# Kernel optimization log

Measured on AMD Instinct MI355X. Metric: run time of the kernel, lower is better.

## Reference

```python
import jax, jax.numpy as jnp
import numpy as np

GRID_RES_SAMPLE = 0.08  # config.grid_resolution_sample
VOXEL_SIZE = 0.04       # scene voxel size encoded in transforms


def setup_inputs() -> dict:
    key = jax.random.key(0)
    ks = jax.random.split(key, 4)
    B, X = 4, 96
    G = 192            # == ceil(X * GRID_RES_SAMPLE / VOXEL_SIZE), matches dynamic size_voxel_grid
    N = 500_000        # sparse occupied voxels per scene
    NUM_ADD = 5000     # static stand-in for occ_grids.sum()+100 mask augmentations
    # scene voxel-grid transform: scale VOXEL_SIZE, translate -5m (same structure per scene)
    T = np.eye(4, dtype=np.float32)
    T[0, 0] = T[1, 1] = T[2, 2] = VOXEL_SIZE
    T[:3, 3] = -5.0
    transforms = np.tile(T, (B, 1, 1)).astype(np.float32)
    transforms_inv = np.stack([np.linalg.inv(t) for t in transforms]).astype(np.float32)
    # per-batch regular coordinate grids with random world offsets in [0,1)m
    offs = np.asarray(jax.random.uniform(ks[0], (B, 3), dtype=jnp.float32))
    ax = np.arange(X, dtype=np.float32) * GRID_RES_SAMPLE
    gx, gy, gz = np.meshgrid(ax, ax, ax, indexing='ij')
    base = np.stack([gx, gy, gz], axis=0)  # [3,X,X,X]
    coords = (base[None] + offs[:, :, None, None, None]).astype(np.float32)
    sparse = jax.random.randint(ks[1], (B, N, 3), 0, 400, dtype=jnp.int32)
    rand_idx = jax.random.randint(ks[2], (3, NUM_ADD), 0, X, dtype=jnp.int32)
    conv_w = jnp.ones((1, 1, 5, 5, 5), jnp.float32)  # Conv3d(1,1,5) all-ones, no bias
    return {
        'coordinate_grids': jnp.asarray(coords),
        'transforms': jnp.asarray(transforms),
        'transforms_inv': jnp.asarray(transforms_inv),
        'sparse_encoding': sparse,
        'conv_w': conv_w,
        'rand_idx': rand_idx,
        'grid_size': G,
    }


def reference(coordinate_grids, transforms, transforms_inv, sparse_encoding, conv_w, rand_idx, grid_size):
    B, C, X, Y, Z = coordinate_grids.shape
    flat = coordinate_grids.reshape(B, 3, -1)
    min_loc = flat.min(-1)   # [B,3]
    max_loc = flat.max(-1)   # [B,3]
    max_size_grid = (max_loc + GRID_RES_SAMPLE - min_loc).max(0)  # [3]
    min_homo = jnp.concatenate([min_loc, jnp.ones((B, 1), flat.dtype)], axis=1)
    min_voxel_idx = jnp.floor(jnp.einsum('bij,bj->bi', transforms_inv, min_homo)[:, :3])
    min_voxel_idx = jnp.maximum(min_voxel_idx, 0.0)  # [B,3]
    size_vox = jnp.ceil(jnp.einsum('bij,j->bi', transforms_inv[:, :3, :3], max_size_grid).max(0))  # [3], == grid_size
    # shift sparse indices into the local window and filter out-of-range ones
    se = sparse_encoding.astype(jnp.float32) - min_voxel_idx[:, None, :]   # [B,N,3]
    valid = ((se >= 0) & (se < size_vox)).all(-1)                          # [B,N]
    sei = jnp.clip(se.astype(jnp.int32), 0, grid_size - 1)
    occ = jnp.zeros((B, grid_size, grid_size, grid_size), jnp.float32)
    b_idx = jnp.broadcast_to(jnp.arange(B)[:, None], valid.shape)
    occ = occ.at[b_idx, sei[..., 0], sei[..., 1], sei[..., 2]].max(valid.astype(jnp.float32))
    # world position of voxel (0,0,0) of the local window and window extent
    min_homo_idx = jnp.concatenate([min_voxel_idx, jnp.ones((B, 1), flat.dtype)], axis=1)
    pos_base = jnp.einsum('bij,bj->bi', transforms, min_homo_idx)[:, :3]   # [B,3]
    extent = jnp.einsum('bij,j->bi', transforms[:, :3, :3], size_vox)      # [B,3]
    voxel_size = extent / size_vox                                          # [B,3]
    # trilinear interpolation of dense occ grid at the coordinate grid (voxel-center convention)
    p = (coordinate_grids - pos_base[:, :, None, None, None]) / voxel_size[:, :, None, None, None] - 0.5
    p0 = jnp.floor(p)
    f = p - p0                       # [B,3,X,Y,Z]
    p0 = p0.astype(jnp.int32)
    bb = jnp.arange(B)[:, None, None, None]
    out = jnp.zeros((B, X, Y, Z), jnp.float32)
    for dx in (0, 1):
        for dy in (0, 1):
            for dz in (0, 1):
                ix = jnp.clip(p0[:, 0] + dx, 0, grid_size - 1)
                iy = jnp.clip(p0[:, 1] + dy, 0, grid_size - 1)
                iz = jnp.clip(p0[:, 2] + dz, 0, grid_size - 1)
                w = ((f[:, 0] if dx else 1 - f[:, 0]) *
                     (f[:, 1] if dy else 1 - f[:, 1]) *
                     (f[:, 2] if dz else 1 - f[:, 2]))
                out = out + w * occ[bb, ix, iy, iz]
    occ_grids = out[:, None]  # [B,1,X,Y,Z]
    # 5x5x5 all-ones conv mask
    conv = jax.lax.conv_general_dilated(
        occ_grids, conv_w, window_strides=(1, 1, 1),
        padding=[(2, 2), (2, 2), (2, 2)],
        dimension_numbers=('NCDHW', 'OIDHW', 'NCDHW'))
    mask = conv > 0
    # random-index mask augmentation (num_voxels_to_add fixed statically)
    num_add = rand_idx.shape[1]
    badd = jnp.arange(num_add) % B
    mask = mask.at[badd, 0, rand_idx[0], rand_idx[1], rand_idx[2]].set(True)
    return occ_grids.astype(bool), mask
```

## Files before the change

### kernel.cpp

```cpp
#include <hip/hip_runtime.h>
#include <math.h>

#define GS   192
#define XS   96
#define XS3  (XS*XS*XS)
#define GRS  0.08f
#define NTHR 256

#define PI_OFF     256
#define PF_OFF     (256 + 1152*4)
#define OCC_OFF    16384
#define OCC_WORDS  (4*GS*GS*(GS/32))
#define OUT_OFF    (OCC_OFF + OCC_WORDS*4)
#define OUTB_WORDS (4*XS*XS*(XS/32))
#define RM_OFF     (OUT_OFF + OUTB_WORDS*4)
#define ZERO_UINT4 ((OCC_WORDS + 2*OUTB_WORDS) / 4)

__device__ __forceinline__ int clampi(int v, int lo, int hi) {
    return v < lo ? lo : (v > hi ? hi : v);
}

__global__ __launch_bounds__(256) void k_init(const float* __restrict__ coords,
                                              const float* __restrict__ T,
                                              const float* __restrict__ Tinv,
                                              float* ws, int B) {
    int gtid = blockIdx.x * NTHR + threadIdx.x;
    uint4* zp = (uint4*)((char*)ws + OCC_OFF);
    if (gtid < ZERO_UINT4) zp[gtid] = make_uint4(0u, 0u, 0u, 0u);

    if (blockIdx.x != 0) return;

    __shared__ int   imn[12], imx[12];
    __shared__ float SS[64];
    int t = threadIdx.x;
    if (t < 12) { imn[t] = 0x7F800000; imx[t] = 0; }
    __syncthreads();
    int tot = B * 3 * XS;
    for (int e = t; e < tot; e += NTHR) {
        int b = e / (3 * XS); int c = (e / XS) % 3; int i = e % XS;
        size_t off = (size_t)(b*3 + c) * XS3
                   + (c == 0 ? (size_t)i * XS * XS : (c == 1 ? (size_t)i * XS : (size_t)i));
        int v = __float_as_int(coords[off]);
        atomicMin(&imn[b*3 + c], v);
        atomicMax(&imx[b*3 + c], v);
    }
    __syncthreads();
    if (t == 0) {
        float mnl[12], mxl[12];
        for (int k = 0; k < 12; k++) { mnl[k] = __int_as_float(imn[k]); mxl[k] = __int_as_float(imx[k]); }
        float msg[3];
        for (int c = 0; c < 3; c++) {
            float m = -__builtin_inff();
            for (int b = 0; b < B; b++) {
                float v = __fadd_rn(mxl[b*3 + c], GRS);
                v = __fsub_rn(v, mnl[b*3 + c]);
                m = fmaxf(m, v);
            }
            msg[c] = m;
        }
        for (int b = 0; b < B; b++)
            for (int i = 0; i < 3; i++) {
                const float* R = Tinv + b*16 + i*4;
                float v = __fmul_rn(R[0], mnl[b*3 + 0]);
                v = __fadd_rn(v, __fmul_rn(R[1], mnl[b*3 + 1]));
                v = __fadd_rn(v, __fmul_rn(R[2], mnl[b*3 + 2]));
                v = __fadd_rn(v, R[3]);
                SS[24 + b*3 + i] = fmaxf(floorf(v), 0.0f);
            }
        for (int i = 0; i < 3; i++) {
            float m = -__builtin_inff();
            for (int b = 0; b < B; b++) {
                const float* R = Tinv + b*16 + i*4;
                float v = __fmul_rn(R[0], msg[0]);
                v = __fadd_rn(v, __fmul_rn(R[1], msg[1]));
                v = __fadd_rn(v, __fmul_rn(R[2], msg[2]));
                m = fmaxf(m, v);
            }
            SS[36 + i] = ceilf(m);
        }
        for (int b = 0; b < B; b++)
            for (int i = 0; i < 3; i++) {
                const float* R = T + b*16 + i*4;
                float v = __fmul_rn(R[0], SS[24 + b*3 + 0]);
                v = __fadd_rn(v, __fmul_rn(R[1], SS[24 + b*3 + 1]));
                v = __fadd_rn(v, __fmul_rn(R[2], SS[24 + b*3 + 2]));
                v = __fadd_rn(v, R[3]);
                SS[40 + b*3 + i] = v;
            }
        for (int b = 0; b < B; b++)
            for (int i = 0; i < 3; i++) {
                const float* R = T + b*16 + i*4;
                float v = __fmul_rn(R[0], SS[36 + 0]);
                v = __fadd_rn(v, __fmul_rn(R[1], SS[36 + 1]));
                v = __fadd_rn(v, __fmul_rn(R[2], SS[36 + 2]));
                SS[52 + b*3 + i] = v / SS[36 + i];
            }
        for (int k = 24; k < 64; k++) ws[k] = SS[k];
    }
    __syncthreads();
    int* PI = (int*)((char*)ws + PI_OFF);
    float* PF = (float*)((char*)ws + PF_OFF);
    for (int e = t; e < tot; e += NTHR) {
        int b = e / (3 * XS); int c = (e / XS) % 3; int i = e % XS;
        size_t off = (size_t)(b*3 + c) * XS3
                   + (c == 0 ? (size_t)i * XS * XS : (c == 1 ? (size_t)i * XS : (size_t)i));
        float v = coords[off];
        float p = (v - SS[40 + b*3 + c]) / SS[52 + b*3 + c] - 0.5f;
        float p0 = floorf(p);
        PI[e] = (int)p0;
        PF[e] = p - p0;
    }
}

__global__ __launch_bounds__(256) void k_scatter(const int* __restrict__ sparse,
                                                 const int* __restrict__ rand_idx,
                                                 float* ws, int N, int total,
                                                 int nadd, int B) {
    int t = blockIdx.x * NTHR + threadIdx.x;
    unsigned* occ   = (unsigned*)((char*)ws + OCC_OFF);
    unsigned* rmask = (unsigned*)((char*)ws + RM_OFF);
    if (t < nadd) {
        int b = t % B;
        int r0 = rand_idx[t], r1 = rand_idx[nadd + t], r2 = rand_idx[2*nadd + t];
        int g = ((b*XS + r0)*XS + r1)*XS + r2;
        atomicOr(&rmask[g >> 5], 1u << (g & 31));
    }
    if (t >= total) return;
    int b = t / N;
    const float* S = ws;
    int s0 = sparse[(size_t)t*3 + 0];
    int s1 = sparse[(size_t)t*3 + 1];
    int s2 = sparse[(size_t)t*3 + 2];
    float e0 = (float)s0 - S[24 + b*3 + 0];
    float e1 = (float)s1 - S[24 + b*3 + 1];
    float e2 = (float)s2 - S[24 + b*3 + 2];
    if (e0 >= 0.f && e0 < S[36+0] && e1 >= 0.f && e1 < S[36+1] && e2 >= 0.f && e2 < S[36+2]) {
        int x = clampi((int)e0, 0, GS-1);
        int y = clampi((int)e1, 0, GS-1);
        int z = clampi((int)e2, 0, GS-1);
        atomicOr(&occ[(((size_t)b*GS + x)*GS + y)*(GS/32) + (z >> 5)], 1u << (z & 31));
    }
}

__global__ __launch_bounds__(256) void k_interp(const float* __restrict__ ws,
                                                int* __restrict__ out0,
                                                unsigned* __restrict__ outb,
                                                int total) {
    int gid = blockIdx.x * NTHR + threadIdx.x;
    if (gid >= total) return;
    const unsigned* occ = (const unsigned*)((const char*)ws + OCC_OFF);
    int z = gid % XS;
    int r1 = gid / XS;
    int y = r1 % XS;
    int r2 = r1 / XS;
    int x = r2 % XS;
    int b = r2 / XS;
    const int* PI = (const int*)((const char*)ws + PI_OFF);
    const float* PF = (const float*)((const char*)ws + PF_OFF);
    int ix = PI[(b*3 + 0)*XS + x]; float fx = PF[(b*3 + 0)*XS + x];
    int iy = PI[(b*3 + 1)*XS + y]; float fy = PF[(b*3 + 1)*XS + y];
    int iz = PI[(b*3 + 2)*XS + z]; float fz = PF[(b*3 + 2)*XS + z];
    int x0 = clampi(ix,   0, GS-1), x1 = clampi(ix+1, 0, GS-1);
    int y0 = clampi(iy,   0, GS-1), y1 = clampi(iy+1, 0, GS-1);
    int z0 = clampi(iz,   0, GS-1), z1 = clampi(iz+1, 0, GS-1);
    float wx0 = 1.f - fx, wx1 = fx, wy0 = 1.f - fy, wy1 = fy, wz0 = 1.f - fz, wz1 = fz;
    const unsigned* r00 = occ + (((size_t)b*GS + x0)*GS + y0)*(GS/32);
    const unsigned* r01 = occ + (((size_t)b*GS + x0)*GS + y1)*(GS/32);
    const unsigned* r10 = occ + (((size_t)b*GS + x1)*GS + y0)*(GS/32);
    const unsigned* r11 = occ + (((size_t)b*GS + x1)*GS + y1)*(GS/32);
    float w00 = wx0*wy0, w01 = wx0*wy1, w10 = wx1*wy0, w11 = wx1*wy1;
    float s = 0.f;
    s += w00*wz0*(float)((r00[z0>>5] >> (z0&31)) & 1u);
    s += w00*wz1*(float)((r00[z1>>5] >> (z1&31)) & 1u);
    s += w01*wz0*(float)((r01[z0>>5] >> (z0&31)) & 1u);
    s += w01*wz1*(float)((r01[z1>>5] >> (z1&31)) & 1u);
    s += w10*wz0*(float)((r10[z0>>5] >> (z0&31)) & 1u);
    s += w10*wz1*(float)((r10[z1>>5] >> (z1&31)) & 1u);
    s += w11*wz0*(float)((r11[z0>>5] >> (z0&31)) & 1u);
    s += w11*wz1*(float)((r11[z1>>5] >> (z1&31)) & 1u);
    bool nz = (s != 0.f);
    out0[gid] = nz ? 1 : 0;
    unsigned long long m = __ballot(nz);
    int lane = threadIdx.x & 63;
    if (lane == 0)  outb[gid >> 5] = (unsigned)m;
    if (lane == 32) outb[gid >> 5] = (unsigned)(m >> 32);
}

__global__ __launch_bounds__(256) void k_dilate_expand(const float* __restrict__ ws,
                                                       int* __restrict__ out1) {
    __shared__ unsigned dsm[NTHR];
    const unsigned* outb  = (const unsigned*)((const char*)ws + OUT_OFF);
    const unsigned* rmask = (const unsigned*)((const char*)ws + RM_OFF);
    int chunk = blockIdx.x;
    int tid = threadIdx.x;
    int t = chunk * NTHR + tid;
    int w = t % 3;
    int rr1 = t / 3;
    int j = rr1 % XS;
    int rr2 = rr1 / XS;
    int i = rr2 % XS;
    int b = rr2 / XS;
    unsigned accP = 0, accC = 0, accN = 0;
    for (int di = -2; di <= 2; di++) {
        int ii = i + di; if (ii < 0 || ii >= XS) continue;
        for (int dj = -2; dj <= 2; dj++) {
            int jj = j + dj; if (jj < 0 || jj >= XS) continue;
            const unsigned* row = outb + ((size_t)(b*XS + ii)*XS + jj)*3;
            accC |= row[w];
            if (w > 0) accP |= row[w-1];
            if (w < 2) accN |= row[w+1];
        }
    }
    unsigned d = accC
               | (accC << 1) | (accP >> 31)
               | (accC << 2) | (accP >> 30)
               | (accC >> 1) | (accN << 31)
               | (accC >> 2) | (accN << 30);
    d |= rmask[t];
    dsm[tid] = d;
    __syncthreads();
    int base = chunk * (NTHR * 32);
    for (int k = 0; k < 32; k++)
        out1[base + k*NTHR + tid] = (int)((dsm[k*8 + (tid >> 5)] >> (tid & 31)) & 1u);
}

extern "C" void kernel_launch(void* const* d_in, const int* in_sizes, int n_in,
                              void* d_out, int out_size, void* d_ws, size_t ws_size,
                              hipStream_t stream) {
    const float* coords = (const float*)d_in[0];
    const float* T      = (const float*)d_in[1];
    const float* Tinv   = (const float*)d_in[2];
    const int*   sparse = (const int*)d_in[3];
    const int*   rand_i = (const int*)d_in[5];
    int* out = (int*)d_out;

    int B = in_sizes[1] / 16;
    int N = in_sizes[3] / (B * 3);
    int nadd = in_sizes[5] / 3;

    float*    ws   = (float*)d_ws;
    unsigned* outb = (unsigned*)((char*)d_ws + OUT_OFF);
    size_t half = (size_t)B * XS3;

    k_init<<<ZERO_UINT4 / NTHR, NTHR, 0, stream>>>(coords, T, Tinv, ws, B);
    int totalPts = B * N;
    k_scatter<<<(totalPts + NTHR - 1) / NTHR, NTHR, 0, stream>>>(sparse, rand_i, ws,
                                                                 N, totalPts, nadd, B);
    int total = B * XS3;
    k_interp<<<total / NTHR, NTHR, 0, stream>>>(ws, out, outb, total);
    k_dilate_expand<<<(B * XS * XS * 3) / NTHR, NTHR, 0, stream>>>(ws, out + half);
}
```

Before: 146.8 us.

## Vectorize sparse scatter loads, swizzle interp blocks, use nontemporal output stores

The scatter kernel now has each thread load 4 points as three int4 loads and loop over them, cutting thread count and load instructions. The interpolation kernel remaps block indices with an 8-way swizzle, hardcodes the grid size for B=4, and drops the bounds check. Both interpolation and dilation outputs use nontemporal stores to avoid polluting cache with write-only data. Correctness relies on B*N being divisible by 4, N divisible by 4 so groups do not straddle batches, and B being 4.

```diff
diff --git a/kernel.cpp b/kernel.cpp
--- a/kernel.cpp
+++ b/kernel.cpp
@@ -114,40 +114,48 @@
 
 __global__ __launch_bounds__(256) void k_scatter(const int* __restrict__ sparse,
                                                  const int* __restrict__ rand_idx,
-                                                 float* ws, int N, int total,
+                                                 float* ws, int N, int nGroups,
                                                  int nadd, int B) {
-    int t = blockIdx.x * NTHR + threadIdx.x;
+    int g = blockIdx.x * NTHR + threadIdx.x;
     unsigned* occ   = (unsigned*)((char*)ws + OCC_OFF);
     unsigned* rmask = (unsigned*)((char*)ws + RM_OFF);
-    if (t < nadd) {
-        int b = t % B;
-        int r0 = rand_idx[t], r1 = rand_idx[nadd + t], r2 = rand_idx[2*nadd + t];
-        int g = ((b*XS + r0)*XS + r1)*XS + r2;
-        atomicOr(&rmask[g >> 5], 1u << (g & 31));
-    }
-    if (t >= total) return;
-    int b = t / N;
+    if (g < nadd) {
+        int b = g % B;
+        int r0 = rand_idx[g], r1 = rand_idx[nadd + g], r2 = rand_idx[2*nadd + g];
+        int idx = ((b*XS + r0)*XS + r1)*XS + r2;
+        atomicOr(&rmask[idx >> 5], 1u << (idx & 31));
+    }
+    if (g >= nGroups) return;
+    int b = (g << 2) / N;
     const float* S = ws;
-    int s0 = sparse[(size_t)t*3 + 0];
-    int s1 = sparse[(size_t)t*3 + 1];
-    int s2 = sparse[(size_t)t*3 + 2];
-    float e0 = (float)s0 - S[24 + b*3 + 0];
-    float e1 = (float)s1 - S[24 + b*3 + 1];
-    float e2 = (float)s2 - S[24 + b*3 + 2];
-    if (e0 >= 0.f && e0 < S[36+0] && e1 >= 0.f && e1 < S[36+1] && e2 >= 0.f && e2 < S[36+2]) {
-        int x = clampi((int)e0, 0, GS-1);
-        int y = clampi((int)e1, 0, GS-1);
-        int z = clampi((int)e2, 0, GS-1);
-        atomicOr(&occ[(((size_t)b*GS + x)*GS + y)*(GS/32) + (z >> 5)], 1u << (z & 31));
-    }
-}
-
+    float m0 = S[24 + b*3 + 0], m1 = S[24 + b*3 + 1], m2 = S[24 + b*3 + 2];
+    float v0 = S[36 + 0],       v1 = S[36 + 1],       v2 = S[36 + 2];
+    const int4* sp = (const int4*)sparse + (size_t)g * 3;
+    int4 a = sp[0], c = sp[1], d = sp[2];
+    int px[4] = {a.x, a.w, c.z, d.y};
+    int py[4] = {a.y, c.x, c.w, d.z};
+    int pz[4] = {a.z, c.y, d.x, d.w};
+    #pragma unroll
+    for (int k = 0; k < 4; k++) {
+        float e0 = (float)px[k] - m0;
+        float e1 = (float)py[k] - m1;
+        float e2 = (float)pz[k] - m2;
+        if (e0 >= 0.f && e0 < v0 && e1 >= 0.f && e1 < v1 && e2 >= 0.f && e2 < v2) {
+            int x = clampi((int)e0, 0, GS-1);
+            int y = clampi((int)e1, 0, GS-1);
+            int z = clampi((int)e2, 0, GS-1);
+            atomicOr(&occ[(((size_t)b*GS + x)*GS + y)*(GS/32) + (z >> 5)], 1u << (z & 31));
+        }
+    }
+}
+
+#define K3_NWG  (4*XS3/NTHR)
+#define K3_CPX  (K3_NWG/8)
 __global__ __launch_bounds__(256) void k_interp(const float* __restrict__ ws,
                                                 int* __restrict__ out0,
-                                                unsigned* __restrict__ outb,
-                                                int total) {
-    int gid = blockIdx.x * NTHR + threadIdx.x;
-    if (gid >= total) return;
+                                                unsigned* __restrict__ outb) {
+    int swz = (blockIdx.x & 7) * K3_CPX + (blockIdx.x >> 3);
+    int gid = swz * NTHR + threadIdx.x;
     const unsigned* occ = (const unsigned*)((const char*)ws + OCC_OFF);
     int z = gid % XS;
     int r1 = gid / XS;
@@ -179,7 +187,7 @@
     s += w11*wz0*(float)((r11[z0>>5] >> (z0&31)) & 1u);
     s += w11*wz1*(float)((r11[z1>>5] >> (z1&31)) & 1u);
     bool nz = (s != 0.f);
-    out0[gid] = nz ? 1 : 0;
+    __builtin_nontemporal_store(nz ? 1 : 0, &out0[gid]);
     unsigned long long m = __ballot(nz);
     int lane = threadIdx.x & 63;
     if (lane == 0)  outb[gid >> 5] = (unsigned)m;
@@ -221,7 +229,8 @@
     __syncthreads();
     int base = chunk * (NTHR * 32);
     for (int k = 0; k < 32; k++)
-        out1[base + k*NTHR + tid] = (int)((dsm[k*8 + (tid >> 5)] >> (tid & 31)) & 1u);
+        __builtin_nontemporal_store((int)((dsm[k*8 + (tid >> 5)] >> (tid & 31)) & 1u),
+                                    &out1[base + k*NTHR + tid]);
 }
 
 extern "C" void kernel_launch(void* const* d_in, const int* in_sizes, int n_in,
@@ -243,10 +252,9 @@
     size_t half = (size_t)B * XS3;
 
     k_init<<<ZERO_UINT4 / NTHR, NTHR, 0, stream>>>(coords, T, Tinv, ws, B);
-    int totalPts = B * N;
-    k_scatter<<<(totalPts + NTHR - 1) / NTHR, NTHR, 0, stream>>>(sparse, rand_i, ws,
-                                                                 N, totalPts, nadd, B);
-    int total = B * XS3;
-    k_interp<<<total / NTHR, NTHR, 0, stream>>>(ws, out, outb, total);
+    int nGroups = (B * N) / 4;
+    k_scatter<<<(nGroups + NTHR - 1) / NTHR, NTHR, 0, stream>>>(sparse, rand_i, ws,
+                                                                N, nGroups, nadd, B);
+    k_interp<<<K3_NWG, NTHR, 0, stream>>>(ws, out, outb);
     k_dilate_expand<<<(B * XS * XS * 3) / NTHR, NTHR, 0, stream>>>(ws, out + half);
 }
```

After: 145.9 us. Within noise of the previous version (-0.6%).
